# Kernel optimization log

Hardware: AMD Instinct MI355X
Metric: run time of the kernel (lower is better)

## Reference

```python
import jax, jax.numpy as jnp
import numpy as np


def _construct_adj(adj, weight_cross_time):
    # adj: (N, N); weight_cross_time: (S-1, N, N) -> local_adj: (S*N, S*N)
    N = adj.shape[0]
    S = weight_cross_time.shape[0] + 1
    local_adj = jnp.zeros((S * N, S * N), dtype=adj.dtype)
    for i in range(S):  # diagonal blocks (small fixed loop over strides)
        local_adj = local_adj.at[i * N:(i + 1) * N, i * N:(i + 1) * N].set(adj)
    for k in range(S - 1):  # cross-time blocks, symmetric placement
        wk = weight_cross_time[k]
        local_adj = local_adj.at[k * N:(k + 1) * N, (k + 1) * N:(k + 2) * N].set(wk)
        local_adj = local_adj.at[(k + 1) * N:(k + 2) * N, k * N:(k + 1) * N].set(wk.T)
    return local_adj


def setup_inputs() -> dict:
    key = jax.random.key(0)
    k1, k2, k3, k4 = jax.random.split(key, 4)
    N, S, B, Cin, Cout = 1024, 3, 32, 64, 64
    # xavier_uniform-like scales for the learned adjacency parameters
    s_adj = float(np.sqrt(6.0 / (N + N)))
    x = jax.random.normal(k1, (S * N, B, Cin), dtype=jnp.float32)
    adj = jax.random.uniform(k2, (N, N), dtype=jnp.float32, minval=-s_adj, maxval=s_adj)
    weight_cross_time = jax.random.uniform(k3, (S - 1, N, N), dtype=jnp.float32, minval=-s_adj, maxval=s_adj)
    s_fc = float(np.sqrt(1.0 / Cin))
    W = jax.random.uniform(k4, (Cin, 2 * Cout), dtype=jnp.float32, minval=-s_fc, maxval=s_fc)
    b = jnp.zeros((2 * Cout,), dtype=jnp.float32)
    return {"x": x, "adj": adj, "weight_cross_time": weight_cross_time, "W": W, "b": b}


def reference(x, adj, weight_cross_time, W, b):
    # Faithful translation of gcn_operation.forward with activation='GLU'.
    Cout = W.shape[-1] // 2
    local_adj = _construct_adj(adj, weight_cross_time)          # (S*N, S*N)
    h = jnp.einsum('nm,mbc->nbc', local_adj, x)                  # (S*N, B, Cin)
    lhs_rhs = h @ W + b                                          # (S*N, B, 2*Cout)
    lhs, rhs = lhs_rhs[..., :Cout], lhs_rhs[..., Cout:]
    return lhs * jax.nn.sigmoid(rhs)                             # (S*N, B, Cout)
```

## Files before the change

kernel.cpp:

```cpp
#include <hip/hip_runtime.h>

typedef unsigned short u16;
typedef unsigned int   u32;
typedef __attribute__((ext_vector_type(8))) short short8;
typedef __attribute__((ext_vector_type(4))) float f32x4;

__device__ __forceinline__ u16 f2bf(float f) {
    u32 u = __float_as_uint(f);
    u = (u + 0x7fffu + ((u >> 16) & 1u)) >> 16;
    return (u16)u;
}

__device__ __forceinline__ void gld_lds16(const void* g, void* l) {
    __builtin_amdgcn_global_load_lds(
        (const __attribute__((address_space(1))) u32*)g,
        (__attribute__((address_space(3))) u32*)l, 16, 0, 0);
}

__device__ __forceinline__ int ridx(int r, int k) {
    return ((((r >> 4) << 7) + (k >> 3)) << 7) + ((r & 15) << 3) + (k & 7);
}

__global__ __launch_bounds__(256) void prep_kernel(
    const float* __restrict__ x, const float* __restrict__ adj,
    const float* __restrict__ wct, const float* __restrict__ W,
    u16* __restrict__ Ab, u16* __restrict__ W0T, u16* __restrict__ W1T,
    u16* __restrict__ Xt, u16* __restrict__ Wt)
{
    __shared__ float tile[64][65];
    const int t = threadIdx.x;
    const int bid = blockIdx.x;

    if (bid < 3072) {
        const int i4 = bid * 256 + t;
        const float4 v = (i4 < 262144) ? ((const float4*)adj)[i4]
                                       : ((const float4*)wct)[i4 - 262144];
        ushort4 o;
        o.x = f2bf(v.x); o.y = f2bf(v.y); o.z = f2bf(v.z); o.w = f2bf(v.w);
        const int m  = i4 >> 18;
        const int lf = i4 & 262143;
        const int r  = lf >> 8;
        const int k  = (lf & 255) << 2;
        *(ushort4*)&Ab[m * 1048576 + ridx(r, k)] = o;
        return;
    }

    const float* src; u16* dst; int C, R, r0, c0, retile;
    if (bid < 3328)      { const int q = bid - 3072; src = wct;           dst = W0T; C = 1024; R = 1024; r0 = (q & 15) << 6; c0 = (q >> 4) << 6; retile = 1; }
    else if (bid < 3584) { const int q = bid - 3328; src = wct + 1048576; dst = W1T; C = 1024; R = 1024; r0 = (q & 15) << 6; c0 = (q >> 4) << 6; retile = 1; }
    else if (bid < 5120) { const int q = bid - 3584; src = x;             dst = Xt;  C = 2048; R = 3072; r0 = (q % 48) << 6; c0 = (q / 48) << 6; retile = 0; }
    else                 { const int q = bid - 5120; src = W;             dst = Wt;  C = 128;  R = 64;   r0 = 0;             c0 = q << 6;        retile = 0; }

#pragma unroll
    for (int it = 0; it < 4; ++it) {
        const int f4 = it * 256 + t;
        const int r  = f4 >> 4;
        const int c4 = (f4 & 15) << 2;
        const float4 v = *(const float4*)&src[(size_t)(r0 + r) * C + c0 + c4];
        tile[r][c4]     = v.x; tile[r][c4 + 1] = v.y;
        tile[r][c4 + 2] = v.z; tile[r][c4 + 3] = v.w;
    }
    __syncthreads();
#pragma unroll
    for (int it = 0; it < 4; ++it) {
        const int f4 = it * 256 + t;
        const int u  = f4 >> 4;
        const int v4 = (f4 & 15) << 2;
        ushort4 o;
        o.x = f2bf(tile[v4][u]);     o.y = f2bf(tile[v4 + 1][u]);
        o.z = f2bf(tile[v4 + 2][u]); o.w = f2bf(tile[v4 + 3][u]);
        if (retile) *(ushort4*)&dst[ridx(c0 + u, r0 + v4)] = o;
        else        *(ushort4*)&dst[(size_t)(c0 + u) * R + r0 + v4] = o;
    }
}

__global__ __launch_bounds__(256, 3) void gemm_h_kernel(
    const u16* __restrict__ Ab,  const u16* __restrict__ W0b,
    const u16* __restrict__ W1b, const u16* __restrict__ W0T,
    const u16* __restrict__ W1T, const u16* __restrict__ Xt,
    const u16* __restrict__ Wt,  const float* __restrict__ bias,
    float* __restrict__ out)
{
    __shared__ u16 Bdb[8192];
    __shared__ u16 Wsm[8192];
    __shared__ float Bias_sm[128];

    const int tid = threadIdx.x;
    const int bid = blockIdx.x;
    const int xcd = bid & 7;
    const int idx = bid >> 3;
    const int i   = idx >> 5;
    const int idp = idx & 31;
    const int nt   = (xcd << 2) + (idp & 3);
    const int row0 = (idp >> 2) << 7;

    const int l    = tid & 63;
    const int w    = tid >> 6;
    const int lrow = l & 15;
    const int g16  = l >> 4;

    {
        u16* wdst = Wsm + (w << 9);
#pragma unroll
        for (int p = 0; p < 4; ++p) {
            const int flat = p * 256 + tid;
            const int row = flat >> 3, slot = flat & 7;
            gld_lds16(Wt + row * 64 + ((slot ^ (row & 7)) << 3), wdst + p * 2048);
        }
        if (tid < 128) Bias_sm[tid] = bias[tid];
    }

    const int brow = tid >> 3;
    const int srck = ((tid & 7) ^ (brow & 7)) << 3;
    auto stageB = [&](u16* buf, const u16* tb, int k0) {
        const u16* g0 = tb + (size_t)brow * 3072 + k0 + srck;
        gld_lds16(g0,             buf + (w << 9));
        gld_lds16(g0 + 32 * 3072, buf + (w << 9) + 2048);
    };

    const int rbw = w << 1;
    auto loadA4 = [&](short8* d, const u16* ta, int k0) {
        const u16* base = ta + (((rbw << 7) + (k0 >> 3)) << 7) + (l << 3);
        d[0] = *(const short8*)(base);
        d[1] = *(const short8*)(base + 512);
        d[2] = *(const short8*)(base + 16384);
        d[3] = *(const short8*)(base + 16384 + 512);
    };

    f32x4 acc[2][4] = {};
    short8 aC[4], aN[4];

    const size_t xbase = (size_t)nt * 64 * 3072;
    const u16 *ca, *cb, *na, *nb, *fa = nullptr, *fb = nullptr;
    int nterms;
    if (i == 0) {
        ca = Ab  + (row0 << 10); cb = Xt + xbase;
        na = W0b + (row0 << 10); nb = Xt + xbase + 1024;
        nterms = 2;
    } else if (i == 1) {
        ca = W0T + (row0 << 10); cb = Xt + xbase;
        na = Ab  + (row0 << 10); nb = Xt + xbase + 1024;
        fa = W1b + (row0 << 10); fb = Xt + xbase + 2048;
        nterms = 3;
    } else {
        ca = W1T + (row0 << 10); cb = Xt + xbase + 1024;
        na = Ab  + (row0 << 10); nb = Xt + xbase + 2048;
        nterms = 2;
    }

    stageB(Bdb, cb, 0);
    loadA4(aC, ca, 0);

    for (int t = 0; t < nterms; ++t) {
#pragma unroll
        for (int k = 0; k < 16; ++k) {
            u16* bufc = Bdb + ((k & 1) << 12);
            u16* bufp = Bdb + (((k + 1) & 1) << 12);
            const u16* pa = (k < 15) ? ca : na;
            const u16* pb = (k < 15) ? cb : nb;
            const int pk0 = (k < 15) ? ((k + 1) << 6) : 0;
            const bool pf = (k < 15) || (na != nullptr);

            __builtin_amdgcn_s_barrier();
            if (pf) {
                stageB(bufp, pb, pk0);
                loadA4(aN, pa, pk0);
                asm volatile("s_waitcnt vmcnt(10)" ::: "memory");
            } else {
                asm volatile("s_waitcnt vmcnt(4)" ::: "memory");
            }
            __builtin_amdgcn_s_barrier();

            short8 bfr[2][4];
#pragma unroll
            for (int kk = 0; kk < 2; ++kk) {
                const int kidx = (kk << 2) | g16;
#pragma unroll
                for (int fn = 0; fn < 4; ++fn) {
                    const int col = (fn << 4) + lrow;
                    bfr[kk][fn] = *(const short8*)&bufc[(col << 6) + ((kidx ^ (col & 7)) << 3)];
                }
            }
#pragma unroll
            for (int kk = 0; kk < 2; ++kk)
#pragma unroll
                for (int fm = 0; fm < 2; ++fm)
#pragma unroll
                    for (int fn = 0; fn < 4; ++fn)
                        acc[fm][fn] = __builtin_amdgcn_mfma_f32_16x16x32_bf16(
                            aC[(fm << 1) | kk], bfr[kk][fn], acc[fm][fn], 0, 0, 0);
#pragma unroll
            for (int j = 0; j < 4; ++j) aC[j] = aN[j];
        }
        ca = na; cb = nb; na = fa; nb = fb; fa = nullptr; fb = nullptr;
    }

    __syncthreads();
    u16* Hsm = Bdb;
#pragma unroll
    for (int fm = 0; fm < 2; ++fm)
#pragma unroll
        for (int fn = 0; fn < 4; ++fn)
#pragma unroll
            for (int r = 0; r < 4; ++r) {
                const int n   = (w << 5) + (fm << 4) + (g16 << 2) + r;
                const int cin = (fn << 4) + lrow;
                Hsm[(n << 6) + (((cin >> 3) ^ (n & 7)) << 3) + (cin & 7)] = f2bf(acc[fm][fn][r]);
            }

    f32x4 acc2[2][8];
#pragma unroll
    for (int fm2 = 0; fm2 < 2; ++fm2)
#pragma unroll
        for (int fn = 0; fn < 8; ++fn) {
            const float bv = Bias_sm[(fn << 4) + lrow];
            acc2[fm2][fn] = (f32x4){bv, bv, bv, bv};
        }
#pragma unroll
    for (int kk = 0; kk < 2; ++kk) {
        const int gg = (kk << 2) | g16;
        short8 ah[2], bw[8];
#pragma unroll
        for (int fm2 = 0; fm2 < 2; ++fm2) {
            const int n = (w << 5) + (fm2 << 4) + lrow;
            ah[fm2] = *(const short8*)&Hsm[(n << 6) + ((gg ^ (n & 7)) << 3)];
        }
#pragma unroll
        for (int fn = 0; fn < 8; ++fn) {
            const int c = (fn << 4) + lrow;
            bw[fn] = *(const short8*)&Wsm[(c << 6) + ((gg ^ (c & 7)) << 3)];
        }
#pragma unroll
        for (int fm2 = 0; fm2 < 2; ++fm2)
#pragma unroll
            for (int fn = 0; fn < 8; ++fn)
                acc2[fm2][fn] = __builtin_amdgcn_mfma_f32_16x16x32_bf16(
                    ah[fm2], bw[fn], acc2[fm2][fn], 0, 0, 0);
    }

    const int n0g = (i << 10) + row0;
#pragma unroll
    for (int fm2 = 0; fm2 < 2; ++fm2)
#pragma unroll
        for (int fn = 0; fn < 4; ++fn)
#pragma unroll
            for (int r = 0; r < 4; ++r) {
                const int nl = (w << 5) + (fm2 << 4) + (g16 << 2) + r;
                const float lhs = acc2[fm2][fn][r];
                const float rhs = acc2[fm2][fn + 4][r];
                const float sg  = 1.0f / (1.0f + __expf(-rhs));
                const int c = (fn << 4) + lrow;
                out[((size_t)(n0g + nl) * 32 + nt) * 64 + c] = lhs * sg;
            }
}

extern "C" void kernel_launch(void* const* d_in, const int* in_sizes, int n_in,
                              void* d_out, int out_size, void* d_ws, size_t ws_size,
                              hipStream_t stream)
{
    const float* x    = (const float*)d_in[0];
    const float* adj  = (const float*)d_in[1];
    const float* wct  = (const float*)d_in[2];
    const float* W    = (const float*)d_in[3];
    const float* bias = (const float*)d_in[4];
    float* out = (float*)d_out;

    char* ws = (char*)d_ws;
    u16* Xt  = (u16*)ws;
    u16* Ab  = (u16*)(ws + 12582912);
    u16* W0b = Ab + 1048576;
    u16* W1b = Ab + 2097152;
    u16* W0T = (u16*)(ws + 18874368);
    u16* W1T = W0T + 1048576;
    u16* Wt  = (u16*)(ws + 23068672);

    prep_kernel<<<5122, 256, 0, stream>>>(x, adj, wct, W, Ab, W0T, W1T, Xt, Wt);
    gemm_h_kernel<<<768, 256, 0, stream>>>(Ab, W0b, W1b, W0T, W1T, Xt, Wt, bias, out);
}
```

Baseline: 63.27 us.

## Double K-tile depth in GEMM mainloop and tile-based prep with fragment-ordered stores

The GEMM main loop now stages 128-wide K tiles instead of 64, which halves the number of barrier-separated iterations per term. It also doubles the LDS B buffer, switches to a 16-way XOR swizzle, loads 8 A fragments per step and raises wave priority around the MFMA block. The prep kernel now converts adj/wct to bf16 through a shared-memory tile, writing contiguous 16-byte fragment runs per thread instead of scattered 8-byte stores, and needs fewer blocks. The costs are more LDS and register use per block, which may lower occupancy under launch_bounds(256,3).

Result: no change. 64.28 us (+1.6%).

```diff
diff --git a/kernel.cpp b/kernel.cpp
--- a/kernel.cpp
+++ b/kernel.cpp
@@ -31,25 +31,26 @@
     const int t = threadIdx.x;
     const int bid = blockIdx.x;
 
-    if (bid < 3072) {
-        const int i4 = bid * 256 + t;
-        const float4 v = (i4 < 262144) ? ((const float4*)adj)[i4]
-                                       : ((const float4*)wct)[i4 - 262144];
-        ushort4 o;
-        o.x = f2bf(v.x); o.y = f2bf(v.y); o.z = f2bf(v.z); o.w = f2bf(v.w);
-        const int m  = i4 >> 18;
-        const int lf = i4 & 262143;
-        const int r  = lf >> 8;
-        const int k  = (lf & 255) << 2;
-        *(ushort4*)&Ab[m * 1048576 + ridx(r, k)] = o;
-        return;
-    }
-
-    const float* src; u16* dst; int C, R, r0, c0, retile;
-    if (bid < 3328)      { const int q = bid - 3072; src = wct;           dst = W0T; C = 1024; R = 1024; r0 = (q & 15) << 6; c0 = (q >> 4) << 6; retile = 1; }
-    else if (bid < 3584) { const int q = bid - 3328; src = wct + 1048576; dst = W1T; C = 1024; R = 1024; r0 = (q & 15) << 6; c0 = (q >> 4) << 6; retile = 1; }
-    else if (bid < 5120) { const int q = bid - 3584; src = x;             dst = Xt;  C = 2048; R = 3072; r0 = (q % 48) << 6; c0 = (q / 48) << 6; retile = 0; }
-    else                 { const int q = bid - 5120; src = W;             dst = Wt;  C = 128;  R = 64;   r0 = 0;             c0 = q << 6;        retile = 0; }
+    const float* src; u16* dst; int C, r0, c0, mode; int R = 0;
+    if (bid < 768) {
+        const int m = bid >> 8, q = bid & 255;
+        src = (m == 0) ? adj : wct + (size_t)(m - 1) * 1048576;
+        dst = Ab + m * 1048576;
+        C = 1024; r0 = (q & 15) << 6; c0 = (q >> 4) << 6; mode = 0;
+    } else if (bid < 1280) {
+        const int mm = (bid - 768) >> 8, q = (bid - 768) & 255;
+        src = wct + (size_t)mm * 1048576;
+        dst = mm ? W1T : W0T;
+        C = 1024; r0 = (q & 15) << 6; c0 = (q >> 4) << 6; mode = 1;
+    } else if (bid < 2816) {
+        const int q = bid - 1280;
+        src = x; dst = Xt; C = 2048; R = 3072;
+        r0 = (q % 48) << 6; c0 = (q / 48) << 6; mode = 2;
+    } else {
+        const int q = bid - 2816;
+        src = W; dst = Wt; C = 128; R = 64;
+        r0 = 0; c0 = q << 6; mode = 2;
+    }
 
 #pragma unroll
     for (int it = 0; it < 4; ++it) {
@@ -61,16 +62,48 @@
         tile[r][c4 + 2] = v.z; tile[r][c4 + 3] = v.w;
     }
     __syncthreads();
-#pragma unroll
-    for (int it = 0; it < 4; ++it) {
-        const int f4 = it * 256 + t;
-        const int u  = f4 >> 4;
-        const int v4 = (f4 & 15) << 2;
-        ushort4 o;
-        o.x = f2bf(tile[v4][u]);     o.y = f2bf(tile[v4 + 1][u]);
-        o.z = f2bf(tile[v4 + 2][u]); o.w = f2bf(tile[v4 + 3][u]);
-        if (retile) *(ushort4*)&dst[ridx(c0 + u, r0 + v4)] = o;
-        else        *(ushort4*)&dst[(size_t)(c0 + u) * R + r0 + v4] = o;
+
+    if (mode == 0) {
+#pragma unroll
+        for (int it = 0; it < 2; ++it) {
+            const int g = it * 256 + t;
+            const int r_lo = g & 15, fragk = (g >> 4) & 7, fragr = g >> 7;
+            const int fi = (((r0 >> 4) + fragr) << 7) + (c0 >> 3) + fragk;
+            const int rr = (fragr << 4) + r_lo, kk = fragk << 3;
+            ushort4 o0, o1;
+            o0.x = f2bf(tile[rr][kk]);     o0.y = f2bf(tile[rr][kk + 1]);
+            o0.z = f2bf(tile[rr][kk + 2]); o0.w = f2bf(tile[rr][kk + 3]);
+            o1.x = f2bf(tile[rr][kk + 4]); o1.y = f2bf(tile[rr][kk + 5]);
+            o1.z = f2bf(tile[rr][kk + 6]); o1.w = f2bf(tile[rr][kk + 7]);
+            *(ushort4*)&dst[(fi << 7) + (r_lo << 3)]     = o0;
+            *(ushort4*)&dst[(fi << 7) + (r_lo << 3) + 4] = o1;
+        }
+    } else if (mode == 1) {
+#pragma unroll
+        for (int it = 0; it < 2; ++it) {
+            const int g = it * 256 + t;
+            const int u_lo = g & 15, fragv = (g >> 4) & 7, fragu = g >> 7;
+            const int fi = (((c0 >> 4) + fragu) << 7) + (r0 >> 3) + fragv;
+            const int uu = (fragu << 4) + u_lo, vv = fragv << 3;
+            ushort4 o0, o1;
+            o0.x = f2bf(tile[vv][uu]);     o0.y = f2bf(tile[vv + 1][uu]);
+            o0.z = f2bf(tile[vv + 2][uu]); o0.w = f2bf(tile[vv + 3][uu]);
+            o1.x = f2bf(tile[vv + 4][uu]); o1.y = f2bf(tile[vv + 5][uu]);
+            o1.z = f2bf(tile[vv + 6][uu]); o1.w = f2bf(tile[vv + 7][uu]);
+            *(ushort4*)&dst[(fi << 7) + (u_lo << 3)]     = o0;
+            *(ushort4*)&dst[(fi << 7) + (u_lo << 3) + 4] = o1;
+        }
+    } else {
+#pragma unroll
+        for (int it = 0; it < 4; ++it) {
+            const int f4 = it * 256 + t;
+            const int u  = f4 >> 4;
+            const int v4 = (f4 & 15) << 2;
+            ushort4 o;
+            o.x = f2bf(tile[v4][u]);     o.y = f2bf(tile[v4 + 1][u]);
+            o.z = f2bf(tile[v4 + 2][u]); o.w = f2bf(tile[v4 + 3][u]);
+            *(ushort4*)&dst[(size_t)(c0 + u) * R + r0 + v4] = o;
+        }
     }
 }
 
@@ -81,7 +114,7 @@
     const u16* __restrict__ Wt,  const float* __restrict__ bias,
     float* __restrict__ out)
 {
-    __shared__ u16 Bdb[8192];
+    __shared__ u16 Bdb[16384];
     __shared__ u16 Wsm[8192];
     __shared__ float Bias_sm[128];
 
@@ -110,25 +143,28 @@
         if (tid < 128) Bias_sm[tid] = bias[tid];
     }
 
-    const int brow = tid >> 3;
-    const int srck = ((tid & 7) ^ (brow & 7)) << 3;
     auto stageB = [&](u16* buf, const u16* tb, int k0) {
-        const u16* g0 = tb + (size_t)brow * 3072 + k0 + srck;
-        gld_lds16(g0,             buf + (w << 9));
-        gld_lds16(g0 + 32 * 3072, buf + (w << 9) + 2048);
+#pragma unroll
+        for (int p = 0; p < 4; ++p) {
+            const int col  = (w << 4) + (p << 2) + g16;
+            const int slog = lrow ^ (col & 15);
+            gld_lds16(tb + (size_t)col * 3072 + k0 + (slog << 3),
+                      buf + (w << 11) + (p << 9));
+        }
     };
 
     const int rbw = w << 1;
-    auto loadA4 = [&](short8* d, const u16* ta, int k0) {
+    auto loadA8 = [&](short8* d, const u16* ta, int k0) {
         const u16* base = ta + (((rbw << 7) + (k0 >> 3)) << 7) + (l << 3);
-        d[0] = *(const short8*)(base);
-        d[1] = *(const short8*)(base + 512);
-        d[2] = *(const short8*)(base + 16384);
-        d[3] = *(const short8*)(base + 16384 + 512);
+#pragma unroll
+        for (int kk = 0; kk < 4; ++kk) {
+            d[kk]     = *(const short8*)(base + (kk << 9));
+            d[kk + 4] = *(const short8*)(base + 16384 + (kk << 9));
+        }
     };
 
     f32x4 acc[2][4] = {};
-    short8 aC[4], aN[4];
+    short8 aC[8], aN[8];
 
     const size_t xbase = (size_t)nt * 64 * 3072;
     const u16 *ca, *cb, *na, *nb, *fa = nullptr, *fb = nullptr;
@@ -149,48 +185,49 @@
     }
 
     stageB(Bdb, cb, 0);
-    loadA4(aC, ca, 0);
+    loadA8(aC, ca, 0);
 
     for (int t = 0; t < nterms; ++t) {
 #pragma unroll
-        for (int k = 0; k < 16; ++k) {
-            u16* bufc = Bdb + ((k & 1) << 12);
-            u16* bufp = Bdb + (((k + 1) & 1) << 12);
-            const u16* pa = (k < 15) ? ca : na;
-            const u16* pb = (k < 15) ? cb : nb;
-            const int pk0 = (k < 15) ? ((k + 1) << 6) : 0;
-            const bool pf = (k < 15) || (na != nullptr);
+        for (int k = 0; k < 8; ++k) {
+            u16* bufc = Bdb + ((k & 1) << 13);
+            u16* bufp = Bdb + (((k + 1) & 1) << 13);
+            const u16* pa = (k < 7) ? ca : na;
+            const u16* pb = (k < 7) ? cb : nb;
+            const int pk0 = (k < 7) ? ((k + 1) << 7) : 0;
+            const bool pf = (k < 7) || (na != nullptr);
 
             __builtin_amdgcn_s_barrier();
             if (pf) {
                 stageB(bufp, pb, pk0);
-                loadA4(aN, pa, pk0);
-                asm volatile("s_waitcnt vmcnt(10)" ::: "memory");
+                loadA8(aN, pa, pk0);
+                asm volatile("s_waitcnt vmcnt(12)" ::: "memory");
             } else {
-                asm volatile("s_waitcnt vmcnt(4)" ::: "memory");
+                asm volatile("s_waitcnt vmcnt(0)" ::: "memory");
             }
             __builtin_amdgcn_s_barrier();
 
-            short8 bfr[2][4];
-#pragma unroll
-            for (int kk = 0; kk < 2; ++kk) {
-                const int kidx = (kk << 2) | g16;
-#pragma unroll
-                for (int fn = 0; fn < 4; ++fn) {
-                    const int col = (fn << 4) + lrow;
-                    bfr[kk][fn] = *(const short8*)&bufc[(col << 6) + ((kidx ^ (col & 7)) << 3)];
-                }
+            __builtin_amdgcn_s_setprio(1);
+#pragma unroll
+            for (int kk = 0; kk < 4; ++kk) {
+                const int so  = ((kk << 2) + g16) ^ lrow;
+                const int cb0 = (lrow << 7) + (so << 3);
+                const short8 b0 = *(const short8*)&bufc[cb0];
+                const short8 b1 = *(const short8*)&bufc[cb0 + 2048];
+                const short8 b2 = *(const short8*)&bufc[cb0 + 4096];
+                const short8 b3 = *(const short8*)&bufc[cb0 + 6144];
+                acc[0][0] = __builtin_amdgcn_mfma_f32_16x16x32_bf16(aC[kk],     b0, acc[0][0], 0, 0, 0);
+                acc[0][1] = __builtin_amdgcn_mfma_f32_16x16x32_bf16(aC[kk],     b1, acc[0][1], 0, 0, 0);
+                acc[0][2] = __builtin_amdgcn_mfma_f32_16x16x32_bf16(aC[kk],     b2, acc[0][2], 0, 0, 0);
+                acc[0][3] = __builtin_amdgcn_mfma_f32_16x16x32_bf16(aC[kk],     b3, acc[0][3], 0, 0, 0);
+                acc[1][0] = __builtin_amdgcn_mfma_f32_16x16x32_bf16(aC[kk + 4], b0, acc[1][0], 0, 0, 0);
+                acc[1][1] = __builtin_amdgcn_mfma_f32_16x16x32_bf16(aC[kk + 4], b1, acc[1][1], 0, 0, 0);
+                acc[1][2] = __builtin_amdgcn_mfma_f32_16x16x32_bf16(aC[kk + 4], b2, acc[1][2], 0, 0, 0);
+                acc[1][3] = __builtin_amdgcn_mfma_f32_16x16x32_bf16(aC[kk + 4], b3, acc[1][3], 0, 0, 0);
             }
-#pragma unroll
-            for (int kk = 0; kk < 2; ++kk)
-#pragma unroll
-                for (int fm = 0; fm < 2; ++fm)
-#pragma unroll
-                    for (int fn = 0; fn < 4; ++fn)
-                        acc[fm][fn] = __builtin_amdgcn_mfma_f32_16x16x32_bf16(
-                            aC[(fm << 1) | kk], bfr[kk][fn], acc[fm][fn], 0, 0, 0);
-#pragma unroll
-            for (int j = 0; j < 4; ++j) aC[j] = aN[j];
+            __builtin_amdgcn_s_setprio(0);
+#pragma unroll
+            for (int j = 0; j < 8; ++j) aC[j] = aN[j];
         }
         ca = na; cb = nb; na = fa; nb = fb; fa = nullptr; fb = nullptr;
     }
@@ -274,6 +311,6 @@
     u16* W1T = W0T + 1048576;
     u16* Wt  = (u16*)(ws + 23068672);
 
-    prep_kernel<<<5122, 256, 0, stream>>>(x, adj, wct, W, Ab, W0T, W1T, Xt, Wt);
+    prep_kernel<<<2818, 256, 0, stream>>>(x, adj, wct, W, Ab, W0T, W1T, Xt, Wt);
     gemm_h_kernel<<<768, 256, 0, stream>>>(Ab, W0b, W1b, W0T, W1T, Xt, Wt, bias, out);
 }
```
